# Performance work log

Measured on AMD Instinct MI355X. Metric: run time of the kernel, lower is better.

## Reference

```python
import jax, jax.numpy as jnp
import numpy as np

B, N, M = 262144, 8, 4  # batch, state_dim, meas_dim
EPS = 1e-6


def _psd(key, b, d, scale=1.0):
    A = jax.random.normal(key, (b, d, d), dtype=jnp.float32)
    return (A @ jnp.swapaxes(A, 1, 2)) / d * scale + 0.1 * jnp.eye(d, dtype=jnp.float32)


def setup_inputs() -> dict:
    key = jax.random.key(0)
    ks = jax.random.split(key, 7)
    x_est = jax.random.normal(ks[0], (B, N, 1), dtype=jnp.float32)
    P_est = _psd(ks[1], B, N)
    F = jnp.eye(N, dtype=jnp.float32) + 0.1 * jax.random.normal(ks[2], (B, N, N), dtype=jnp.float32)
    Q = _psd(ks[3], B, N, scale=0.1)
    z = jax.random.normal(ks[4], (B, M, 1), dtype=jnp.float32)
    H = jax.random.normal(ks[5], (B, M, N), dtype=jnp.float32)
    R = _psd(ks[6], B, M, scale=0.5)
    return {"x_est": x_est, "P_est": P_est, "F": F, "Q": Q, "z": z, "H": H, "R": R}


def reference(x_est, P_est, F, Q, z, H, R):
    # Predict: x_pred = F x, P_pred = F P F^T + Q
    x_pred = F @ x_est                                     # [B,n,1]
    P_pred = F @ P_est @ jnp.swapaxes(F, 1, 2) + Q         # [B,n,n]
    # Update
    H_T = jnp.swapaxes(H, 1, 2)                            # [B,n,m]
    S = H @ P_pred @ H_T + R + EPS * jnp.eye(M, dtype=P_pred.dtype)  # [B,m,m]
    S_inv = jnp.linalg.inv(S)
    K = P_pred @ H_T @ S_inv                               # [B,n,m]
    y = z - H @ x_pred                                     # innovation [B,m,1]
    x_new = x_pred + K @ y
    IKH = jnp.eye(N, dtype=P_pred.dtype) - K @ H           # [B,n,n]
    P_new = IKH @ P_pred
    return x_new, P_new, K
```

## Files before the change

### kernel.cpp

```cpp
#include <hip/hip_runtime.h>


#define EPS 1e-6f
#define SYMIDX(r, c) ((r) * ((r) + 1) / 2 + (c))

__device__ __forceinline__ void gl_lds16(const float* g, float* l) {
    __builtin_amdgcn_global_load_lds(
        (const __attribute__((address_space(1))) void*)(uintptr_t)g,
        (__attribute__((address_space(3))) void*)(unsigned)(uintptr_t)l,
        16, 0, 0);
}

__device__ __forceinline__ void stage64(const float* __restrict__ src, int gstart,
                                        float* ldsbase, int lane, int B) {
#pragma unroll
    for (int i = 0; i < 16; ++i) {
        int b = i * 4 + (lane >> 4);
        int e = lane & 15;
        int gb = gstart + b;
        if (gb > B - 1) gb = B - 1;
        gl_lds16(src + (size_t)gb * 64 + (size_t)((e ^ (b & 7)) * 4),
                 ldsbase + i * 256);
    }
}

__global__ __launch_bounds__(64) __attribute__((amdgpu_waves_per_eu(1)))
void kf_kernel(const float* __restrict__ x_est,
               const float* __restrict__ P_est,
               const float* __restrict__ Fin,
               const float* __restrict__ Qin,
               const float* __restrict__ zin,
               const float* __restrict__ Hin,
               const float* __restrict__ Rin,
               float* __restrict__ out, int B) {
    const int lane = threadIdx.x;
    const int ngroups = (B + 63) >> 6;
    int g = blockIdx.x;
    if (g >= ngroups) return;
    const int stride = gridDim.x;

    __shared__ __align__(16) float lds[12288];

    stage64(Fin, g * 64, lds, lane, B);
    stage64(P_est, g * 64, lds + 4096, lane, B);
    stage64(Qin, g * 64, lds + 8192, lane, B);
    int bc = g * 64 + lane;
    if (bc > B - 1) bc = B - 1;
    float4 zz = reinterpret_cast<const float4*>(zin)[bc];
    float4 xa = reinterpret_cast<const float4*>(x_est)[2 * bc];
    float4 xb = reinterpret_cast<const float4*>(x_est)[2 * bc + 1];
    asm volatile("s_waitcnt vmcnt(0)" ::: "memory");

    while (true) {
        const int b0 = g * 64 + lane;
        const bool full = (g * 64 + 64 <= B);
        const int sw = lane & 7;
        const float4* L4 = reinterpret_cast<const float4*>(lds);
        const int gn = g + stride;
        const int gnc = (gn < ngroups) ? gn : 0;

        int b0c = (b0 > B - 1) ? B - 1 : b0;
        float Hm[32];
        {
            const float4* H4 = reinterpret_cast<const float4*>(Hin + (size_t)b0c * 32);
#pragma unroll
            for (int i = 0; i < 8; ++i) {
                float4 h = H4[i];
                Hm[4 * i + 0] = h.x; Hm[4 * i + 1] = h.y; Hm[4 * i + 2] = h.z; Hm[4 * i + 3] = h.w;
            }
        }
        const float4* Rp = reinterpret_cast<const float4*>(Rin + (size_t)b0c * 16);
        float4 r0 = Rp[0], r1 = Rp[1], r2 = Rp[2], r3 = Rp[3];
        int bcn = gnc * 64 + lane;
        if (bcn > B - 1) bcn = B - 1;
        float4 zzn = reinterpret_cast<const float4*>(zin)[bcn];
        float4 xan = reinterpret_cast<const float4*>(x_est)[2 * bcn];
        float4 xbn = reinterpret_cast<const float4*>(x_est)[2 * bcn + 1];

        float Fr[64];
#pragma unroll
        for (int r = 0; r < 8; ++r) {
            float4 a = L4[lane * 16 + ((2 * r) ^ sw)];
            float4 c = L4[lane * 16 + ((2 * r + 1) ^ sw)];
            Fr[r * 8 + 0] = a.x; Fr[r * 8 + 1] = a.y; Fr[r * 8 + 2] = a.z; Fr[r * 8 + 3] = a.w;
            Fr[r * 8 + 4] = c.x; Fr[r * 8 + 5] = c.y; Fr[r * 8 + 6] = c.z; Fr[r * 8 + 7] = c.w;
        }
        float Ps[36];
#pragma unroll
        for (int r = 0; r < 8; ++r) {
            float4 a = L4[1024 + lane * 16 + ((2 * r) ^ sw)];
            float rw[4] = {a.x, a.y, a.z, a.w};
            if (r < 4) {
#pragma unroll
                for (int j = 0; j < 4; ++j)
                    if (j <= r) Ps[SYMIDX(r, j)] = rw[j];
            } else {
                float4 c = L4[1024 + lane * 16 + ((2 * r + 1) ^ sw)];
                float rw2[4] = {c.x, c.y, c.z, c.w};
#pragma unroll
                for (int j = 0; j < 4; ++j) Ps[SYMIDX(r, j)] = rw[j];
#pragma unroll
                for (int j = 4; j < 8; ++j)
                    if (j <= r) Ps[SYMIDX(r, j)] = rw2[j - 4];
            }
        }
        float Qs[36];
#pragma unroll
        for (int r = 0; r < 8; ++r) {
            float4 a = L4[2048 + lane * 16 + ((2 * r) ^ sw)];
            float rw[4] = {a.x, a.y, a.z, a.w};
            if (r < 4) {
#pragma unroll
                for (int j = 0; j < 4; ++j)
                    if (j <= r) Qs[SYMIDX(r, j)] = rw[j];
            } else {
                float4 c = L4[2048 + lane * 16 + ((2 * r + 1) ^ sw)];
                float rw2[4] = {c.x, c.y, c.z, c.w};
#pragma unroll
                for (int j = 0; j < 4; ++j) Qs[SYMIDX(r, j)] = rw[j];
#pragma unroll
                for (int j = 4; j < 8; ++j)
                    if (j <= r) Qs[SYMIDX(r, j)] = rw2[j - 4];
            }
        }
        asm volatile("s_waitcnt lgkmcnt(0)" ::: "memory");

        stage64(Fin, gnc * 64, lds, lane, B);
        stage64(P_est, gnc * 64, lds + 4096, lane, B);
        stage64(Qin, gnc * 64, lds + 8192, lane, B);
        asm volatile("" ::: "memory");

        float xp[8];
        {
            float x[8] = {xa.x, xa.y, xa.z, xa.w, xb.x, xb.y, xb.z, xb.w};
#pragma unroll
            for (int i = 0; i < 8; ++i) {
                float s = 0.f;
#pragma unroll
                for (int j = 0; j < 8; ++j) s += Fr[i * 8 + j] * x[j];
                xp[i] = s;
            }
        }

        float Pps[36];
#pragma unroll
        for (int i = 0; i < 8; ++i) {
            float Ti[8];
#pragma unroll
            for (int j = 0; j < 8; ++j) {
                float s = 0.f;
#pragma unroll
                for (int k = 0; k < 8; ++k) {
                    float pkj = (k >= j) ? Ps[SYMIDX(k, j)] : Ps[SYMIDX(j, k)];
                    s += Fr[i * 8 + k] * pkj;
                }
                Ti[j] = s;
            }
#pragma unroll
            for (int j = 0; j <= i; ++j) {
                float s = Qs[SYMIDX(i, j)];
#pragma unroll
                for (int k = 0; k < 8; ++k) s += Ti[k] * Fr[j * 8 + k];
                Pps[SYMIDX(i, j)] = s;
            }
        }

        float HP[32];
#pragma unroll
        for (int i = 0; i < 4; ++i)
#pragma unroll
            for (int j = 0; j < 8; ++j) {
                float s = 0.f;
#pragma unroll
                for (int k = 0; k < 8; ++k) {
                    float pkj = (k >= j) ? Pps[SYMIDX(k, j)] : Pps[SYMIDX(j, k)];
                    s += Hm[i * 8 + k] * pkj;
                }
                HP[i * 8 + j] = s;
            }

        float y[4];
        {
            float zv[4] = {zz.x, zz.y, zz.z, zz.w};
#pragma unroll
            for (int i = 0; i < 4; ++i) {
                float s = zv[i];
#pragma unroll
                for (int k = 0; k < 8; ++k) s -= Hm[i * 8 + k] * xp[k];
                y[i] = s;
            }
        }

        float S[16];
        {
            float Rr[16] = {r0.x, r0.y, r0.z, r0.w, r1.x, r1.y, r1.z, r1.w,
                            r2.x, r2.y, r2.z, r2.w, r3.x, r3.y, r3.z, r3.w};
#pragma unroll
            for (int i = 0; i < 4; ++i)
#pragma unroll
                for (int j = 0; j < 4; ++j) {
                    float s = Rr[i * 4 + j];
#pragma unroll
                    for (int k = 0; k < 8; ++k) s += HP[i * 8 + k] * Hm[j * 8 + k];
                    if (i == j) s += EPS;
                    S[i * 4 + j] = s;
                }
        }

        float inv[16];
        inv[0]  =  S[5]*S[10]*S[15] - S[5]*S[11]*S[14] - S[9]*S[6]*S[15] + S[9]*S[7]*S[14] + S[13]*S[6]*S[11] - S[13]*S[7]*S[10];
        inv[4]  = -S[4]*S[10]*S[15] + S[4]*S[11]*S[14] + S[8]*S[6]*S[15] - S[8]*S[7]*S[14] - S[12]*S[6]*S[11] + S[12]*S[7]*S[10];
        inv[8]  =  S[4]*S[9]*S[15]  - S[4]*S[11]*S[13] - S[8]*S[5]*S[15] + S[8]*S[7]*S[13] + S[12]*S[5]*S[11] - S[12]*S[7]*S[9];
        inv[12] = -S[4]*S[9]*S[14]  + S[4]*S[10]*S[13] + S[8]*S[5]*S[14] - S[8]*S[6]*S[13] - S[12]*S[5]*S[10] + S[12]*S[6]*S[9];
        inv[1]  = -S[1]*S[10]*S[15] + S[1]*S[11]*S[14] + S[9]*S[2]*S[15] - S[9]*S[3]*S[14] - S[13]*S[2]*S[11] + S[13]*S[3]*S[10];
        inv[5]  =  S[0]*S[10]*S[15] - S[0]*S[11]*S[14] - S[8]*S[2]*S[15] + S[8]*S[3]*S[14] + S[12]*S[2]*S[11] - S[12]*S[3]*S[10];
        inv[9]  = -S[0]*S[9]*S[15]  + S[0]*S[11]*S[13] + S[8]*S[1]*S[15] - S[8]*S[3]*S[13] - S[12]*S[1]*S[11] + S[12]*S[3]*S[9];
        inv[13] =  S[0]*S[9]*S[14]  - S[0]*S[10]*S[13] - S[8]*S[1]*S[14] + S[8]*S[2]*S[13] + S[12]*S[1]*S[10] - S[12]*S[2]*S[9];
        inv[2]  =  S[1]*S[6]*S[15]  - S[1]*S[7]*S[14]  - S[5]*S[2]*S[15] + S[5]*S[3]*S[14] + S[13]*S[2]*S[7]  - S[13]*S[3]*S[6];
        inv[6]  = -S[0]*S[6]*S[15]  + S[0]*S[7]*S[14]  + S[4]*S[2]*S[15] - S[4]*S[3]*S[14] - S[12]*S[2]*S[7]  + S[12]*S[3]*S[6];
        inv[10] =  S[0]*S[5]*S[15]  - S[0]*S[7]*S[13]  - S[4]*S[1]*S[15] + S[4]*S[3]*S[13] + S[12]*S[1]*S[7]  - S[12]*S[3]*S[5];
        inv[14] = -S[0]*S[5]*S[14]  + S[0]*S[6]*S[13]  + S[4]*S[1]*S[14] - S[4]*S[2]*S[13] - S[12]*S[1]*S[6]  + S[12]*S[2]*S[5];
        inv[3]  = -S[1]*S[6]*S[11]  + S[1]*S[7]*S[10]  + S[5]*S[2]*S[11] - S[5]*S[3]*S[10] - S[9]*S[2]*S[7]   + S[9]*S[3]*S[6];
        inv[7]  =  S[0]*S[6]*S[11]  - S[0]*S[7]*S[10]  - S[4]*S[2]*S[11] + S[4]*S[3]*S[10] + S[8]*S[2]*S[7]   - S[8]*S[3]*S[6];
        inv[11] = -S[0]*S[5]*S[11]  + S[0]*S[7]*S[9]   + S[4]*S[1]*S[11] - S[4]*S[3]*S[9]  - S[8]*S[1]*S[7]   + S[8]*S[3]*S[5];
        inv[15] =  S[0]*S[5]*S[10]  - S[0]*S[6]*S[9]   - S[4]*S[1]*S[10] + S[4]*S[2]*S[9]  + S[8]*S[1]*S[6]   - S[8]*S[2]*S[5];
        float det = S[0]*inv[0] + S[1]*inv[4] + S[2]*inv[8] + S[3]*inv[12];
        float rdet = 1.0f / det;
#pragma unroll
        for (int i = 0; i < 16; ++i) inv[i] *= rdet;

        float K[32];
#pragma unroll
        for (int i = 0; i < 8; ++i)
#pragma unroll
            for (int j = 0; j < 4; ++j) {
                float s = 0.f;
#pragma unroll
                for (int k = 0; k < 4; ++k) s += HP[k * 8 + i] * inv[k * 4 + j];
                K[i * 4 + j] = s;
            }

        auto doStores = [&]() {
            float4* xo = reinterpret_cast<float4*>(out + (size_t)b0 * 8);
            float xn[8];
#pragma unroll
            for (int i = 0; i < 8; ++i) {
                float s = xp[i];
#pragma unroll
                for (int k = 0; k < 4; ++k) s += K[i * 4 + k] * y[k];
                xn[i] = s;
            }
            xo[0] = make_float4(xn[0], xn[1], xn[2], xn[3]);
            xo[1] = make_float4(xn[4], xn[5], xn[6], xn[7]);

            float4* po = reinterpret_cast<float4*>(out + (size_t)B * 8 + (size_t)b0 * 64);
#pragma unroll
            for (int i = 0; i < 8; ++i) {
                float r[8];
#pragma unroll
                for (int j = 0; j < 8; ++j) {
                    float pij = (i >= j) ? Pps[SYMIDX(i, j)] : Pps[SYMIDX(j, i)];
                    float s = pij;
#pragma unroll
                    for (int k = 0; k < 4; ++k) s -= K[i * 4 + k] * HP[k * 8 + j];
                    r[j] = s;
                }
                po[2 * i + 0] = make_float4(r[0], r[1], r[2], r[3]);
                po[2 * i + 1] = make_float4(r[4], r[5], r[6], r[7]);
            }

            float4* ko = reinterpret_cast<float4*>(out + (size_t)B * 72 + (size_t)b0 * 32);
#pragma unroll
            for (int i = 0; i < 8; ++i)
                ko[i] = make_float4(K[4 * i + 0], K[4 * i + 1], K[4 * i + 2], K[4 * i + 3]);
        };

        if (full) {
            doStores();
            asm volatile("s_waitcnt vmcnt(26)" ::: "memory");
        } else {
            if (b0 < B) doStores();
            asm volatile("s_waitcnt vmcnt(0)" ::: "memory");
        }

        if (gn >= ngroups) break;
        g = gn;
        zz = zzn; xa = xan; xb = xbn;
    }
}

extern "C" void kernel_launch(void* const* d_in, const int* in_sizes, int n_in,
                              void* d_out, int out_size, void* d_ws, size_t ws_size,
                              hipStream_t stream) {
    const float* x_est = (const float*)d_in[0];
    const float* P_est = (const float*)d_in[1];
    const float* F     = (const float*)d_in[2];
    const float* Q     = (const float*)d_in[3];
    const float* z     = (const float*)d_in[4];
    const float* H     = (const float*)d_in[5];
    const float* R     = (const float*)d_in[6];
    float* out = (float*)d_out;
    int B = in_sizes[0] / 8;
    int ngroups = (B + 63) / 64;
    int grid = ngroups < 768 ? ngroups : 768;
    kf_kernel<<<grid, 64, 0, stream>>>(x_est, P_est, F, Q, z, H, R, out, B);
}
```

Baseline: 310.9 us.

## Load Q lower triangle directly from global, shrink LDS, raise occupancy

Q is no longer staged into LDS through async global-to-LDS copies. Each lane instead reads only the float4 chunks of its own Q matrix that hold the lower triangle, which cuts the LDS buffer from 48 KB to 32 KB. The waves-per-EU hint goes from 1 to 2 and the persistent grid grows from 768 to 1280 blocks to use the extra occupancy. The software prefetch of z and x for the next group is dropped; they are now loaded in the current iteration. The risks are register spilling under the tighter per-wave budget, and per-lane strided Q reads with worse coalescing and less latency hiding.

```diff
diff --git a/kernel.cpp b/kernel.cpp
--- a/kernel.cpp
+++ b/kernel.cpp
@@ -24,7 +24,7 @@
     }
 }
 
-__global__ __launch_bounds__(64) __attribute__((amdgpu_waves_per_eu(1)))
+__global__ __launch_bounds__(64) __attribute__((amdgpu_waves_per_eu(2)))
 void kf_kernel(const float* __restrict__ x_est,
                const float* __restrict__ P_est,
                const float* __restrict__ Fin,
@@ -39,16 +39,10 @@
     if (g >= ngroups) return;
     const int stride = gridDim.x;
 
-    __shared__ __align__(16) float lds[12288];
+    __shared__ __align__(16) float lds[8192];
 
     stage64(Fin, g * 64, lds, lane, B);
     stage64(P_est, g * 64, lds + 4096, lane, B);
-    stage64(Qin, g * 64, lds + 8192, lane, B);
-    int bc = g * 64 + lane;
-    if (bc > B - 1) bc = B - 1;
-    float4 zz = reinterpret_cast<const float4*>(zin)[bc];
-    float4 xa = reinterpret_cast<const float4*>(x_est)[2 * bc];
-    float4 xb = reinterpret_cast<const float4*>(x_est)[2 * bc + 1];
     asm volatile("s_waitcnt vmcnt(0)" ::: "memory");
 
     while (true) {
@@ -59,24 +53,6 @@
         const int gn = g + stride;
         const int gnc = (gn < ngroups) ? gn : 0;
 
-        int b0c = (b0 > B - 1) ? B - 1 : b0;
-        float Hm[32];
-        {
-            const float4* H4 = reinterpret_cast<const float4*>(Hin + (size_t)b0c * 32);
-#pragma unroll
-            for (int i = 0; i < 8; ++i) {
-                float4 h = H4[i];
-                Hm[4 * i + 0] = h.x; Hm[4 * i + 1] = h.y; Hm[4 * i + 2] = h.z; Hm[4 * i + 3] = h.w;
-            }
-        }
-        const float4* Rp = reinterpret_cast<const float4*>(Rin + (size_t)b0c * 16);
-        float4 r0 = Rp[0], r1 = Rp[1], r2 = Rp[2], r3 = Rp[3];
-        int bcn = gnc * 64 + lane;
-        if (bcn > B - 1) bcn = B - 1;
-        float4 zzn = reinterpret_cast<const float4*>(zin)[bcn];
-        float4 xan = reinterpret_cast<const float4*>(x_est)[2 * bcn];
-        float4 xbn = reinterpret_cast<const float4*>(x_est)[2 * bcn + 1];
-
         float Fr[64];
 #pragma unroll
         for (int r = 0; r < 8; ++r) {
@@ -104,30 +80,47 @@
                     if (j <= r) Ps[SYMIDX(r, j)] = rw2[j - 4];
             }
         }
+        asm volatile("s_waitcnt lgkmcnt(0)" ::: "memory");
+
+        int b0c = (b0 > B - 1) ? B - 1 : b0;
         float Qs[36];
-#pragma unroll
-        for (int r = 0; r < 8; ++r) {
-            float4 a = L4[2048 + lane * 16 + ((2 * r) ^ sw)];
-            float rw[4] = {a.x, a.y, a.z, a.w};
-            if (r < 4) {
-#pragma unroll
-                for (int j = 0; j < 4; ++j)
-                    if (j <= r) Qs[SYMIDX(r, j)] = rw[j];
-            } else {
-                float4 c = L4[2048 + lane * 16 + ((2 * r + 1) ^ sw)];
-                float rw2[4] = {c.x, c.y, c.z, c.w};
-#pragma unroll
-                for (int j = 0; j < 4; ++j) Qs[SYMIDX(r, j)] = rw[j];
-#pragma unroll
-                for (int j = 4; j < 8; ++j)
-                    if (j <= r) Qs[SYMIDX(r, j)] = rw2[j - 4];
-            }
-        }
-        asm volatile("s_waitcnt lgkmcnt(0)" ::: "memory");
+        {
+            const float4* Q4 = reinterpret_cast<const float4*>(Qin + (size_t)b0c * 64);
+            float4 q0 = Q4[0], q2 = Q4[2], q4 = Q4[4], q6 = Q4[6];
+            float4 q8 = Q4[8], q9 = Q4[9], q10 = Q4[10], q11 = Q4[11];
+            float4 q12 = Q4[12], q13 = Q4[13], q14 = Q4[14], q15 = Q4[15];
+            Qs[SYMIDX(0,0)] = q0.x;
+            Qs[SYMIDX(1,0)] = q2.x;  Qs[SYMIDX(1,1)] = q2.y;
+            Qs[SYMIDX(2,0)] = q4.x;  Qs[SYMIDX(2,1)] = q4.y;  Qs[SYMIDX(2,2)] = q4.z;
+            Qs[SYMIDX(3,0)] = q6.x;  Qs[SYMIDX(3,1)] = q6.y;  Qs[SYMIDX(3,2)] = q6.z;  Qs[SYMIDX(3,3)] = q6.w;
+            Qs[SYMIDX(4,0)] = q8.x;  Qs[SYMIDX(4,1)] = q8.y;  Qs[SYMIDX(4,2)] = q8.z;  Qs[SYMIDX(4,3)] = q8.w;
+            Qs[SYMIDX(4,4)] = q9.x;
+            Qs[SYMIDX(5,0)] = q10.x; Qs[SYMIDX(5,1)] = q10.y; Qs[SYMIDX(5,2)] = q10.z; Qs[SYMIDX(5,3)] = q10.w;
+            Qs[SYMIDX(5,4)] = q11.x; Qs[SYMIDX(5,5)] = q11.y;
+            Qs[SYMIDX(6,0)] = q12.x; Qs[SYMIDX(6,1)] = q12.y; Qs[SYMIDX(6,2)] = q12.z; Qs[SYMIDX(6,3)] = q12.w;
+            Qs[SYMIDX(6,4)] = q13.x; Qs[SYMIDX(6,5)] = q13.y; Qs[SYMIDX(6,6)] = q13.z;
+            Qs[SYMIDX(7,0)] = q14.x; Qs[SYMIDX(7,1)] = q14.y; Qs[SYMIDX(7,2)] = q14.z; Qs[SYMIDX(7,3)] = q14.w;
+            Qs[SYMIDX(7,4)] = q15.x; Qs[SYMIDX(7,5)] = q15.y; Qs[SYMIDX(7,6)] = q15.z; Qs[SYMIDX(7,7)] = q15.w;
+        }
+        float Hm[32];
+        {
+            const float4* H4 = reinterpret_cast<const float4*>(Hin + (size_t)b0c * 32);
+#pragma unroll
+            for (int i = 0; i < 8; ++i) {
+                float4 h = H4[i];
+                Hm[4 * i + 0] = h.x; Hm[4 * i + 1] = h.y; Hm[4 * i + 2] = h.z; Hm[4 * i + 3] = h.w;
+            }
+        }
+        const float4* Rp = reinterpret_cast<const float4*>(Rin + (size_t)b0c * 16);
+        float4 r0 = Rp[0], r1 = Rp[1], r2 = Rp[2], r3 = Rp[3];
+        float4 zz = reinterpret_cast<const float4*>(zin)[b0c];
+        float4 xa = reinterpret_cast<const float4*>(x_est)[2 * b0c];
+        float4 xb = reinterpret_cast<const float4*>(x_est)[2 * b0c + 1];
+
+        asm volatile("" ::: "memory");
 
         stage64(Fin, gnc * 64, lds, lane, B);
         stage64(P_est, gnc * 64, lds + 4096, lane, B);
-        stage64(Qin, gnc * 64, lds + 8192, lane, B);
         asm volatile("" ::: "memory");
 
         float xp[8];
@@ -285,7 +278,6 @@
 
         if (gn >= ngroups) break;
         g = gn;
-        zz = zzn; xa = xan; xb = xbn;
     }
 }
 
@@ -302,6 +294,6 @@
     float* out = (float*)d_out;
     int B = in_sizes[0] / 8;
     int ngroups = (B + 63) / 64;
-    int grid = ngroups < 768 ? ngroups : 768;
+    int grid = ngroups < 1280 ? ngroups : 1280;
     kf_kernel<<<grid, 64, 0, stream>>>(x_est, P_est, F, Q, z, H, R, out, B);
 }
```

Measured after the change: 391.7 us. 1.26x slower.
